# Performance work log

Measured on AMD Instinct MI355X. Metric: run time of the kernel, lower is better.

## Reference

```python
import jax, jax.numpy as jnp
import numpy as np

NEG_SLOPE = 0.2  # PyG GATConv default


def gat_conv(x, src, dst, W, att_src, att_dst, bias, n_nodes):
    # x: [N, F_in]; W: [F_in, H*C]; att_*: [H, C]; bias: [H*C]
    H, C = att_src.shape
    h = (x @ W).reshape(n_nodes, H, C)                      # [N, H, C]
    a_src = jnp.sum(h * att_src, axis=-1)                   # [N, H]
    a_dst = jnp.sum(h * att_dst, axis=-1)                   # [N, H]
    e = jax.nn.leaky_relu(a_src[src] + a_dst[dst], NEG_SLOPE)  # [E, H]
    # segment softmax over incoming edges of each dst node
    e_max = jax.ops.segment_max(e, dst, num_segments=n_nodes)
    e_max = jnp.where(jnp.isfinite(e_max), e_max, 0.0)
    ex = jnp.exp(e - e_max[dst])                             # [E, H]
    denom = jax.ops.segment_sum(ex, dst, num_segments=n_nodes)
    alpha = ex / (denom[dst] + 1e-16)                        # [E, H]
    msg = h[src] * alpha[:, :, None]                         # [E, H, C]
    out = jax.ops.segment_sum(msg, dst, num_segments=n_nodes)  # [N, H, C]
    return out.reshape(n_nodes, H * C) + bias


def setup_inputs() -> dict:
    key = jax.random.key(0)
    ks = jax.random.split(key, 12)
    N, F_in, Hd, heads, F_out, E = 50000, 128, 32, 8, 16, 800000
    x = jax.random.normal(ks[0], (N, F_in), dtype=jnp.float32)
    edge_index = jax.random.randint(ks[1], (2, E), 0, N, dtype=jnp.int64)
    g = 0.1
    return {
        "x": x,
        "edge_index": edge_index,
        "W1": jax.random.normal(ks[2], (F_in, heads * Hd), dtype=jnp.float32) * g,
        "att_src1": jax.random.normal(ks[3], (heads, Hd), dtype=jnp.float32) * g,
        "att_dst1": jax.random.normal(ks[4], (heads, Hd), dtype=jnp.float32) * g,
        "b1": jnp.zeros((heads * Hd,), dtype=jnp.float32),
        "W2": jax.random.normal(ks[5], (heads * Hd, Hd), dtype=jnp.float32) * g,
        "att_src2": jax.random.normal(ks[6], (1, Hd), dtype=jnp.float32) * g,
        "att_dst2": jax.random.normal(ks[7], (1, Hd), dtype=jnp.float32) * g,
        "b2": jnp.zeros((Hd,), dtype=jnp.float32),
        "Wout": jax.random.normal(ks[8], (Hd, F_out), dtype=jnp.float32) * g,
        "bout": jnp.zeros((F_out,), dtype=jnp.float32),
    }


def reference(x, edge_index, W1, att_src1, att_dst1, b1, W2, att_src2, att_dst2, b2, Wout, bout):
    N = x.shape[0]
    # PyG GATConv adds self loops by default
    loops = jnp.arange(N, dtype=edge_index.dtype)
    src = jnp.concatenate([edge_index[0], loops])
    dst = jnp.concatenate([edge_index[1], loops])
    h = jax.nn.elu(gat_conv(x, src, dst, W1, att_src1, att_dst1, b1, N))
    # dropout is identity in eval mode
    h = jax.nn.elu(gat_conv(h, src, dst, W2, att_src2, att_dst2, b2, N))
    return h @ Wout + bout
```

## Files before the change

### kernel.cpp

```cpp
#include <hip/hip_runtime.h>
#include <math.h>

#define NEG_SLOPE 0.2f

typedef __attribute__((ext_vector_type(8))) short bfrag8;
typedef __attribute__((ext_vector_type(4))) float f4acc;

__device__ __forceinline__ float bflo(unsigned int u) {
  union { unsigned int i; float f; } c;
  c.i = u << 16;
  return c.f;
}
__device__ __forceinline__ float bfhi(unsigned int u) {
  union { unsigned int i; float f; } c;
  c.i = u & 0xFFFF0000u;
  return c.f;
}
__device__ __forceinline__ unsigned short f2bf(float f) {
  union { float f; unsigned int i; } c;
  c.f = f;
  unsigned int i = c.i;
  return (unsigned short)((i + 0x7FFFu + ((i >> 16) & 1u)) >> 16);
}


__global__ __launch_bounds__(256) void hist_kernel(const int* __restrict__ ei,
                                                   int* __restrict__ counts, int e) {
  int i = blockIdx.x * 256 + threadIdx.x;
  if (i < e) atomicAdd(&counts[ei[e + i]], 1);
}

#define SCAN_TILE 2048
__global__ __launch_bounds__(256) void scan1_kernel(const int* __restrict__ counts,
                                                    int* __restrict__ offsets,
                                                    int* __restrict__ bsum, int n) {
  __shared__ int wtot[4];
  int tid = threadIdx.x;
  int base = blockIdx.x * SCAN_TILE + tid * 8;
  int v[8];
#pragma unroll
  for (int k = 0; k < 8; ++k) v[k] = (base + k < n) ? counts[base + k] + 1 : 0;
#pragma unroll
  for (int k = 1; k < 8; ++k) v[k] += v[k - 1];
  int tsum = v[7];
  int lane = tid & 63;
  int w = tid >> 6;
  int ws = tsum;
#pragma unroll
  for (int off = 1; off < 64; off <<= 1) {
    int t = __shfl_up(ws, off, 64);
    if (lane >= off) ws += t;
  }
  if (lane == 63) wtot[w] = ws;
  __syncthreads();
  int woff = 0;
#pragma unroll
  for (int k = 0; k < 3; ++k)
    if (k < w) woff += wtot[k];
  int thrBase = woff + ws - tsum;
#pragma unroll
  for (int k = 0; k < 8; ++k)
    if (base + k < n) offsets[base + k] = thrBase + v[k];
  if (tid == 255) bsum[blockIdx.x] = woff + ws;
}

__global__ __launch_bounds__(256) void scan3_kernel(const int* __restrict__ counts,
                                                    int* __restrict__ offsets,
                                                    const int* __restrict__ bsum,
                                                    int* __restrict__ cursor,
                                                    int n, int nb) {
  __shared__ int pres[64];
  int tid = threadIdx.x;
  if (tid < 64) {
    int v = (tid < nb) ? bsum[tid] : 0;
#pragma unroll
    for (int off = 1; off < 64; off <<= 1) {
      int t = __shfl_up(v, off, 64);
      if ((tid & 63) >= off) v += t;
    }
    pres[tid] = v;
  }
  __syncthreads();
  int i = blockIdx.x * 256 + tid;
  if (i > n) return;
  if (i == n) {
    offsets[n] = pres[nb - 1];
    return;
  }
  int b = i >> 11;
  int pre = (b == 0) ? 0 : pres[b - 1];
  int excl = pre + offsets[i] - (counts[i] + 1);
  offsets[i] = excl;
  cursor[i] = excl;
}

__global__ __launch_bounds__(256) void fill_kernel(const int* __restrict__ ei,
                                                   int* __restrict__ cursor,
                                                   int* __restrict__ csr, int n, int e) {
  int i = blockIdx.x * 256 + threadIdx.x;
  if (i < e) {
    int s = ei[i];
    int d = ei[e + i];
    int pos = atomicAdd(&cursor[d], 1);
    csr[pos] = s;
  } else if (i < e + n) {
    int node = i - e;
    int pos = atomicAdd(&cursor[node], 1);
    csr[pos] = node;
  } else if (i < e + n + 64) {
    csr[i] = 0;
  }
}


__global__ __launch_bounds__(256) void wcast_kernel(const float* __restrict__ W1,
                                                    const float* __restrict__ W2,
                                                    unsigned short* __restrict__ w1t,
                                                    unsigned short* __restrict__ w2t) {
  int gid = blockIdx.x * 256 + threadIdx.x;
#pragma unroll
  for (int u = 0; u < 4; ++u) {
    int j = gid * 4 + u;
    if (j < 128 * 256) {
      int k = j >> 8, c = j & 255;
      w1t[c * 128 + k] = f2bf(W1[j]);
    } else if (j < 128 * 256 + 256 * 32) {
      int j2 = j - 128 * 256;
      int k = j2 >> 5, c = j2 & 31;
      w2t[c * 256 + k] = f2bf(W2[j2]);
    }
  }
}

__global__ __launch_bounds__(256) void xcast_kernel(const float* __restrict__ x,
                                                    unsigned short* __restrict__ xb,
                                                    int total) {
  int gid = blockIdx.x * 256 + threadIdx.x;
  int i = gid * 8;
  if (i >= total) return;
  float4 v0 = *(const float4*)(x + i);
  float4 v1 = *(const float4*)(x + i + 4);
  uint4 q;
  q.x = (unsigned int)f2bf(v0.x) | ((unsigned int)f2bf(v0.y) << 16);
  q.y = (unsigned int)f2bf(v0.z) | ((unsigned int)f2bf(v0.w) << 16);
  q.z = (unsigned int)f2bf(v1.x) | ((unsigned int)f2bf(v1.y) << 16);
  q.w = (unsigned int)f2bf(v1.z) | ((unsigned int)f2bf(v1.w) << 16);
  *(uint4*)(xb + i) = q;
}


__global__ __launch_bounds__(256) void gemm1_kernel(const unsigned short* __restrict__ xb,
                                                    const unsigned short* __restrict__ w1t,
                                                    const float* __restrict__ att_src,
                                                    const float* __restrict__ att_dst,
                                                    unsigned short* __restrict__ h1b,
                                                    float* __restrict__ as1,
                                                    float* __restrict__ ad1, int n) {
  int tid = threadIdx.x;
  int wave = tid >> 6, lane = tid & 63;
  int quad = lane >> 4, l16 = lane & 15;
  int row0 = blockIdx.x * 64 + wave * 16;
  int col0 = blockIdx.y * 128;
  int rowA = min(row0 + l16, n - 1);

  f4acc acc[8];
#pragma unroll
  for (int t = 0; t < 8; ++t) acc[t] = (f4acc)(0.f);

#pragma unroll
  for (int kc = 0; kc < 4; ++kc) {
    bfrag8 a = *(const bfrag8*)(xb + (size_t)rowA * 128 + kc * 32 + quad * 8);
#pragma unroll
    for (int t = 0; t < 8; ++t) {
      bfrag8 b = *(const bfrag8*)(w1t + (size_t)(col0 + t * 16 + l16) * 128 + kc * 32 + quad * 8);
      acc[t] = __builtin_amdgcn_mfma_f32_16x16x32_bf16(a, b, acc[t], 0, 0, 0);
    }
  }

#pragma unroll
  for (int r = 0; r < 4; ++r) {
    int gr = row0 + quad * 4 + r;
    if (gr < n) {
#pragma unroll
      for (int t = 0; t < 8; ++t)
        h1b[(size_t)gr * 256 + col0 + t * 16 + l16] = f2bf(acc[t][r]);
    }
  }

  float s1[4][4], s2[4][4];
#pragma unroll
  for (int r = 0; r < 4; ++r)
#pragma unroll
    for (int hl = 0; hl < 4; ++hl) { s1[r][hl] = 0.f; s2[r][hl] = 0.f; }
#pragma unroll
  for (int t = 0; t < 8; ++t) {
    float av = att_src[col0 + t * 16 + l16];
    float dv = att_dst[col0 + t * 16 + l16];
    int hl = t >> 1;
#pragma unroll
    for (int r = 0; r < 4; ++r) {
      s1[r][hl] += acc[t][r] * av;
      s2[r][hl] += acc[t][r] * dv;
    }
  }
#pragma unroll
  for (int r = 0; r < 4; ++r) {
#pragma unroll
    for (int hl = 0; hl < 4; ++hl) {
      float v1 = s1[r][hl], v2 = s2[r][hl];
      v1 += __shfl_xor(v1, 1); v1 += __shfl_xor(v1, 2);
      v1 += __shfl_xor(v1, 4); v1 += __shfl_xor(v1, 8);
      v2 += __shfl_xor(v2, 1); v2 += __shfl_xor(v2, 2);
      v2 += __shfl_xor(v2, 4); v2 += __shfl_xor(v2, 8);
      if (l16 == 0) {
        int gr = row0 + quad * 4 + r;
        if (gr < n) {
          int hg = (col0 >> 5) + hl;
          as1[(size_t)gr * 8 + hg] = v1;
          ad1[(size_t)gr * 8 + hg] = v2;
        }
      }
    }
  }
}


__global__ __launch_bounds__(256) void agg1_kernel(const unsigned short* __restrict__ h1b,
                                                   const float* __restrict__ as1,
                                                   const float* __restrict__ ad1,
                                                   const int* __restrict__ offsets,
                                                   const int* __restrict__ csr,
                                                   const float* __restrict__ bias,
                                                   unsigned short* __restrict__ h1ob, int n) {
  __shared__ float peLds[4 * 64 * 8];
  int gtid = blockIdx.x * 256 + threadIdx.x;
  int node = gtid >> 6;
  int lane = gtid & 63;
  if (node >= n) return;
  float* myPe = peLds + (threadIdx.x >> 6) * 512;
  int beg = offsets[node], end = offsets[node + 1];
  int deg = end - beg;
  int half = lane >> 5, sub = lane & 31, head = sub >> 2;

  float4 adv0 = ((const float4*)(ad1 + (size_t)node * 8))[0];
  float4 adv1 = ((const float4*)(ad1 + (size_t)node * 8))[1];
  float ad_[8] = {adv0.x, adv0.y, adv0.z, adv0.w, adv1.x, adv1.y, adv1.z, adv1.w};

  float l = 0.f;
  float a[8] = {};

  for (int c0 = 0; c0 < deg; c0 += 64) {
    int cnt = min(64, deg - c0);
    bool valid = (c0 + lane) < deg;
    int s = csr[beg + c0 + lane];
    {
      const float4* ap = (const float4*)(as1 + (size_t)s * 8);
      float4 r0 = ap[0], r1 = ap[1];
      float asv[8] = {r0.x, r0.y, r0.z, r0.w, r1.x, r1.y, r1.z, r1.w};
      float pv[8];
#pragma unroll
      for (int h = 0; h < 8; ++h) {
        float ev = asv[h] + ad_[h];
        ev = ev > 0.f ? ev : NEG_SLOPE * ev;
        pv[h] = valid ? __expf(ev) : 0.f;
      }
      *(float4*)&myPe[lane * 8 + 0] = make_float4(pv[0], pv[1], pv[2], pv[3]);
      *(float4*)&myPe[lane * 8 + 4] = make_float4(pv[4], pv[5], pv[6], pv[7]);
    }
#pragma unroll 2
    for (int j = 0; j < cnt; j += 2) {
      int e = j + half;
      int s2 = csr[beg + c0 + e];
      float pe = myPe[e * 8 + head];
      l += pe;
      uint4 hv = *(const uint4*)(h1b + (size_t)s2 * 256 + sub * 8);
      a[0] += pe * bflo(hv.x);
      a[1] += pe * bfhi(hv.x);
      a[2] += pe * bflo(hv.y);
      a[3] += pe * bfhi(hv.y);
      a[4] += pe * bflo(hv.z);
      a[5] += pe * bfhi(hv.z);
      a[6] += pe * bflo(hv.w);
      a[7] += pe * bfhi(hv.w);
    }
  }
  l += __shfl_xor(l, 32);
#pragma unroll
  for (int i = 0; i < 8; ++i) a[i] += __shfl_xor(a[i], 32);

  if (half == 0) {
    float inv = 1.f / (l + 1e-16f);
    const float4* bp = (const float4*)(bias + sub * 8);
    float4 b0 = bp[0], b1 = bp[1];
    float o[8];
    o[0] = a[0] * inv + b0.x;
    o[1] = a[1] * inv + b0.y;
    o[2] = a[2] * inv + b0.z;
    o[3] = a[3] * inv + b0.w;
    o[4] = a[4] * inv + b1.x;
    o[5] = a[5] * inv + b1.y;
    o[6] = a[6] * inv + b1.z;
    o[7] = a[7] * inv + b1.w;
    unsigned int q[4];
#pragma unroll
    for (int j = 0; j < 4; ++j) {
      float e0 = o[j * 2], e1 = o[j * 2 + 1];
      e0 = e0 > 0.f ? e0 : expm1f(e0);
      e1 = e1 > 0.f ? e1 : expm1f(e1);
      q[j] = (unsigned int)f2bf(e0) | ((unsigned int)f2bf(e1) << 16);
    }
    *(uint4*)(h1ob + (size_t)node * 256 + sub * 8) = make_uint4(q[0], q[1], q[2], q[3]);
  }
}


__global__ __launch_bounds__(256) void gemm2_kernel(const unsigned short* __restrict__ h1ob,
                                                    const unsigned short* __restrict__ w2t,
                                                    const float* __restrict__ att_src,
                                                    const float* __restrict__ att_dst,
                                                    unsigned short* __restrict__ h2b,
                                                    float* __restrict__ as2,
                                                    float* __restrict__ ad2, int n) {
  int tid = threadIdx.x;
  int wave = tid >> 6, lane = tid & 63;
  int quad = lane >> 4, l16 = lane & 15;
  int row0 = blockIdx.x * 64 + wave * 16;
  int rowA = min(row0 + l16, n - 1);

  f4acc acc[2];
  acc[0] = (f4acc)(0.f);
  acc[1] = (f4acc)(0.f);

#pragma unroll
  for (int kc = 0; kc < 8; ++kc) {
    bfrag8 a = *(const bfrag8*)(h1ob + (size_t)rowA * 256 + kc * 32 + quad * 8);
#pragma unroll
    for (int t = 0; t < 2; ++t) {
      bfrag8 b = *(const bfrag8*)(w2t + (size_t)(t * 16 + l16) * 256 + kc * 32 + quad * 8);
      acc[t] = __builtin_amdgcn_mfma_f32_16x16x32_bf16(a, b, acc[t], 0, 0, 0);
    }
  }

#pragma unroll
  for (int r = 0; r < 4; ++r) {
    int gr = row0 + quad * 4 + r;
    if (gr < n) {
      h2b[(size_t)gr * 32 + l16] = f2bf(acc[0][r]);
      h2b[(size_t)gr * 32 + 16 + l16] = f2bf(acc[1][r]);
    }
  }

  float s1[4], s2v[4];
#pragma unroll
  for (int r = 0; r < 4; ++r) { s1[r] = 0.f; s2v[r] = 0.f; }
#pragma unroll
  for (int t = 0; t < 2; ++t) {
    float av = att_src[t * 16 + l16];
    float dv = att_dst[t * 16 + l16];
#pragma unroll
    for (int r = 0; r < 4; ++r) {
      s1[r] += acc[t][r] * av;
      s2v[r] += acc[t][r] * dv;
    }
  }
#pragma unroll
  for (int r = 0; r < 4; ++r) {
    float v1 = s1[r], v2 = s2v[r];
    v1 += __shfl_xor(v1, 1); v1 += __shfl_xor(v1, 2);
    v1 += __shfl_xor(v1, 4); v1 += __shfl_xor(v1, 8);
    v2 += __shfl_xor(v2, 1); v2 += __shfl_xor(v2, 2);
    v2 += __shfl_xor(v2, 4); v2 += __shfl_xor(v2, 8);
    if (l16 == 0) {
      int gr = row0 + quad * 4 + r;
      if (gr < n) {
        as2[gr] = v1;
        ad2[gr] = v2;
      }
    }
  }
}


__global__ __launch_bounds__(256) void agg2_kernel(const unsigned short* __restrict__ h2b,
                                                   const float* __restrict__ as2,
                                                   const float* __restrict__ ad2,
                                                   const int* __restrict__ offsets,
                                                   const int* __restrict__ csr,
                                                   const float* __restrict__ bias,
                                                   const float* __restrict__ Wout,
                                                   const float* __restrict__ bout,
                                                   float* __restrict__ out, int n) {
  __shared__ float peLds[4 * 64];
  __shared__ float wLds[512];
  __shared__ float hrow[4][32];
  int tid = threadIdx.x;
  wLds[tid] = Wout[tid];
  wLds[tid + 256] = Wout[tid + 256];
  __syncthreads();

  int gtid = blockIdx.x * 256 + tid;
  int node = gtid >> 6;
  int lane = gtid & 63;
  if (node >= n) return;
  int wv = tid >> 6;
  float* myPe = peLds + wv * 64;
  float ad = ad2[node];
  int beg = offsets[node], end = offsets[node + 1];
  int deg = end - beg;
  int quarter = lane >> 4;
  int dsub = lane & 15;

  float l = 0.f, a0 = 0.f, a1 = 0.f;
  for (int c0 = 0; c0 < deg; c0 += 64) {
    int cnt = min(64, deg - c0);
    bool valid = (c0 + lane) < deg;
    int s = csr[beg + c0 + lane];
    float ev = as2[s] + ad;
    ev = ev > 0.f ? ev : NEG_SLOPE * ev;
    myPe[lane] = valid ? __expf(ev) : 0.f;
#pragma unroll 2
    for (int j = 0; j < cnt; j += 4) {
      int e = j + quarter;
      int s2 = csr[beg + c0 + e];
      float pe = myPe[e];
      l += pe;
      unsigned int hv = *(const unsigned int*)(h2b + (size_t)s2 * 32 + dsub * 2);
      a0 += pe * bflo(hv);
      a1 += pe * bfhi(hv);
    }
  }
  l += __shfl_xor(l, 16);
  l += __shfl_xor(l, 32);
  a0 += __shfl_xor(a0, 16);
  a1 += __shfl_xor(a1, 16);
  a0 += __shfl_xor(a0, 32);
  a1 += __shfl_xor(a1, 32);
  if (lane < 16) {
    float inv = 1.f / (l + 1e-16f);
    float o0 = a0 * inv + bias[dsub * 2];
    float o1 = a1 * inv + bias[dsub * 2 + 1];
    o0 = o0 > 0.f ? o0 : expm1f(o0);
    o1 = o1 > 0.f ? o1 : expm1f(o1);
    hrow[wv][dsub * 2] = o0;
    hrow[wv][dsub * 2 + 1] = o1;
  }
  if (lane < 16) {
    float s = bout[lane];
#pragma unroll
    for (int c = 0; c < 32; ++c) s += hrow[wv][c] * wLds[c * 16 + lane];
    out[(size_t)node * 16 + lane] = s;
  }
}


extern "C" void kernel_launch(void* const* d_in, const int* in_sizes, int n_in,
                              void* d_out, int out_size, void* d_ws, size_t ws_size,
                              hipStream_t stream) {
  const float* x        = (const float*)d_in[0];
  const int*   ei       = (const int*)d_in[1];
  const float* W1       = (const float*)d_in[2];
  const float* att_src1 = (const float*)d_in[3];
  const float* att_dst1 = (const float*)d_in[4];
  const float* b1       = (const float*)d_in[5];
  const float* W2       = (const float*)d_in[6];
  const float* att_src2 = (const float*)d_in[7];
  const float* att_dst2 = (const float*)d_in[8];
  const float* b2       = (const float*)d_in[9];
  const float* Wout     = (const float*)d_in[10];
  const float* bout     = (const float*)d_in[11];
  float* out = (float*)d_out;

  int n = in_sizes[0] / 128;
  int e = in_sizes[1] / 2;

  char* w = (char*)d_ws;
  unsigned short* h1b  = (unsigned short*)w; w += (size_t)n * 256 * 2;
  unsigned short* h1ob = (unsigned short*)w; w += (size_t)n * 256 * 2;
  unsigned short* xb   = (unsigned short*)w; w += (size_t)n * 128 * 2;
  unsigned short* h2b  = (unsigned short*)w; w += (size_t)n * 32 * 2;
  unsigned short* w1t  = (unsigned short*)w; w += (size_t)256 * 128 * 2;
  unsigned short* w2t  = (unsigned short*)w; w += (size_t)32 * 256 * 2;
  float* as1  = (float*)w; w += (size_t)n * 8 * 4;
  float* ad1  = (float*)w; w += (size_t)n * 8 * 4;
  float* as2  = (float*)w; w += (size_t)n * 4;
  float* ad2  = (float*)w; w += (size_t)n * 4;
  int* counts  = (int*)w; w += (size_t)n * 4;
  int* offsets = (int*)w; w += (size_t)(n + 16) * 4;
  int* cursor  = (int*)w; w += (size_t)n * 4;
  int* csr     = (int*)w; w += (size_t)(e + n + 64) * 4;
  int* bsum    = (int*)w; w += (size_t)256 * 4;

  int nb = (n + SCAN_TILE - 1) / SCAN_TILE;

  hipMemsetAsync(counts, 0, (size_t)n * 4, stream);
  hist_kernel<<<(e + 255) / 256, 256, 0, stream>>>(ei, counts, e);
  scan1_kernel<<<nb, 256, 0, stream>>>(counts, offsets, bsum, n);
  scan3_kernel<<<(n + 256) / 256, 256, 0, stream>>>(counts, offsets, bsum, cursor, n, nb);
  fill_kernel<<<(e + n + 64 + 255) / 256, 256, 0, stream>>>(ei, cursor, csr, n, e);

  wcast_kernel<<<40, 256, 0, stream>>>(W1, W2, w1t, w2t);
  xcast_kernel<<<(n * 128 / 8 + 255) / 256, 256, 0, stream>>>(x, xb, n * 128);

  gemm1_kernel<<<dim3((n + 63) / 64, 2), 256, 0, stream>>>(xb, w1t, att_src1, att_dst1,
                                                           h1b, as1, ad1, n);
  agg1_kernel<<<(n + 3) / 4, 256, 0, stream>>>(h1b, as1, ad1, offsets, csr, b1, h1ob, n);

  gemm2_kernel<<<(n + 63) / 64, 256, 0, stream>>>(h1ob, w2t, att_src2, att_dst2,
                                                  h2b, as2, ad2, n);
  agg2_kernel<<<(n + 3) / 4, 256, 0, stream>>>(h2b, as2, ad2, offsets, csr, b2,
                                               Wout, bout, out, n);
}
```

Baseline: 342.7 us.

## Fuse histogram and cast kernels, raise aggregation unroll, use fast ELU

Merges the degree histogram, the x-to-bf16 cast and the weight transpose-cast into one prep kernel, removing two kernel launches and letting the independent work overlap. Raises the unroll factor of the edge-gather loops in both aggregation kernels from 2 to 4 to keep more loads in flight. Replaces expm1f-based ELU with __expf(x)-1, which is cheaper but loses accuracy for small negative inputs. The larger unroll may raise register pressure in the aggregation kernels.

```diff
diff --git a/kernel.cpp b/kernel.cpp
--- a/kernel.cpp
+++ b/kernel.cpp
@@ -22,13 +22,53 @@
   unsigned int i = c.i;
   return (unsigned short)((i + 0x7FFFu + ((i >> 16) & 1u)) >> 16);
 }
-
-
-__global__ __launch_bounds__(256) void hist_kernel(const int* __restrict__ ei,
-                                                   int* __restrict__ counts, int e) {
-  int i = blockIdx.x * 256 + threadIdx.x;
-  if (i < e) atomicAdd(&counts[ei[e + i]], 1);
-}
+__device__ __forceinline__ float elu(float x) { return x > 0.f ? x : __expf(x) - 1.f; }
+
+
+__global__ __launch_bounds__(256) void prep_kernel(const int* __restrict__ ei,
+                                                   int* __restrict__ counts,
+                                                   const float* __restrict__ x,
+                                                   const float* __restrict__ W1,
+                                                   const float* __restrict__ W2,
+                                                   unsigned short* __restrict__ xb,
+                                                   unsigned short* __restrict__ w1t,
+                                                   unsigned short* __restrict__ w2t,
+                                                   int e, int xThreads, int totalx) {
+  int gid = blockIdx.x * 256 + threadIdx.x;
+  if (gid < e) {
+    atomicAdd(&counts[ei[e + gid]], 1);
+    return;
+  }
+  int g1 = gid - e;
+  if (g1 < xThreads) {
+    int i = g1 * 8;
+    if (i < totalx) {
+      float4 v0 = *(const float4*)(x + i);
+      float4 v1 = *(const float4*)(x + i + 4);
+      uint4 q;
+      q.x = (unsigned int)f2bf(v0.x) | ((unsigned int)f2bf(v0.y) << 16);
+      q.y = (unsigned int)f2bf(v0.z) | ((unsigned int)f2bf(v0.w) << 16);
+      q.z = (unsigned int)f2bf(v1.x) | ((unsigned int)f2bf(v1.y) << 16);
+      q.w = (unsigned int)f2bf(v1.z) | ((unsigned int)f2bf(v1.w) << 16);
+      *(uint4*)(xb + i) = q;
+    }
+    return;
+  }
+  int g2 = g1 - xThreads;
+#pragma unroll
+  for (int u = 0; u < 4; ++u) {
+    int j = g2 * 4 + u;
+    if (j < 128 * 256) {
+      int k = j >> 8, c = j & 255;
+      w1t[c * 128 + k] = f2bf(W1[j]);
+    } else if (j < 128 * 256 + 256 * 32) {
+      int j2 = j - 128 * 256;
+      int k = j2 >> 5, c = j2 & 31;
+      w2t[c * 256 + k] = f2bf(W2[j2]);
+    }
+  }
+}
+
 
 #define SCAN_TILE 2048
 __global__ __launch_bounds__(256) void scan1_kernel(const int* __restrict__ counts,
@@ -110,42 +150,6 @@
   } else if (i < e + n + 64) {
     csr[i] = 0;
   }
-}
-
-
-__global__ __launch_bounds__(256) void wcast_kernel(const float* __restrict__ W1,
-                                                    const float* __restrict__ W2,
-                                                    unsigned short* __restrict__ w1t,
-                                                    unsigned short* __restrict__ w2t) {
-  int gid = blockIdx.x * 256 + threadIdx.x;
-#pragma unroll
-  for (int u = 0; u < 4; ++u) {
-    int j = gid * 4 + u;
-    if (j < 128 * 256) {
-      int k = j >> 8, c = j & 255;
-      w1t[c * 128 + k] = f2bf(W1[j]);
-    } else if (j < 128 * 256 + 256 * 32) {
-      int j2 = j - 128 * 256;
-      int k = j2 >> 5, c = j2 & 31;
-      w2t[c * 256 + k] = f2bf(W2[j2]);
-    }
-  }
-}
-
-__global__ __launch_bounds__(256) void xcast_kernel(const float* __restrict__ x,
-                                                    unsigned short* __restrict__ xb,
-                                                    int total) {
-  int gid = blockIdx.x * 256 + threadIdx.x;
-  int i = gid * 8;
-  if (i >= total) return;
-  float4 v0 = *(const float4*)(x + i);
-  float4 v1 = *(const float4*)(x + i + 4);
-  uint4 q;
-  q.x = (unsigned int)f2bf(v0.x) | ((unsigned int)f2bf(v0.y) << 16);
-  q.y = (unsigned int)f2bf(v0.z) | ((unsigned int)f2bf(v0.w) << 16);
-  q.z = (unsigned int)f2bf(v1.x) | ((unsigned int)f2bf(v1.y) << 16);
-  q.w = (unsigned int)f2bf(v1.z) | ((unsigned int)f2bf(v1.w) << 16);
-  *(uint4*)(xb + i) = q;
 }
 
 
@@ -267,7 +271,7 @@
       *(float4*)&myPe[lane * 8 + 0] = make_float4(pv[0], pv[1], pv[2], pv[3]);
       *(float4*)&myPe[lane * 8 + 4] = make_float4(pv[4], pv[5], pv[6], pv[7]);
     }
-#pragma unroll 2
+#pragma unroll 4
     for (int j = 0; j < cnt; j += 2) {
       int e = j + half;
       int s2 = csr[beg + c0 + e];
@@ -293,22 +297,18 @@
     const float4* bp = (const float4*)(bias + sub * 8);
     float4 b0 = bp[0], b1 = bp[1];
     float o[8];
-    o[0] = a[0] * inv + b0.x;
-    o[1] = a[1] * inv + b0.y;
-    o[2] = a[2] * inv + b0.z;
-    o[3] = a[3] * inv + b0.w;
-    o[4] = a[4] * inv + b1.x;
-    o[5] = a[5] * inv + b1.y;
-    o[6] = a[6] * inv + b1.z;
-    o[7] = a[7] * inv + b1.w;
+    o[0] = elu(a[0] * inv + b0.x);
+    o[1] = elu(a[1] * inv + b0.y);
+    o[2] = elu(a[2] * inv + b0.z);
+    o[3] = elu(a[3] * inv + b0.w);
+    o[4] = elu(a[4] * inv + b1.x);
+    o[5] = elu(a[5] * inv + b1.y);
+    o[6] = elu(a[6] * inv + b1.z);
+    o[7] = elu(a[7] * inv + b1.w);
     unsigned int q[4];
 #pragma unroll
-    for (int j = 0; j < 4; ++j) {
-      float e0 = o[j * 2], e1 = o[j * 2 + 1];
-      e0 = e0 > 0.f ? e0 : expm1f(e0);
-      e1 = e1 > 0.f ? e1 : expm1f(e1);
-      q[j] = (unsigned int)f2bf(e0) | ((unsigned int)f2bf(e1) << 16);
-    }
+    for (int j = 0; j < 4; ++j)
+      q[j] = (unsigned int)f2bf(o[j * 2]) | ((unsigned int)f2bf(o[j * 2 + 1]) << 16);
     *(uint4*)(h1ob + (size_t)node * 256 + sub * 8) = make_uint4(q[0], q[1], q[2], q[3]);
   }
 }
@@ -418,7 +418,7 @@
     float ev = as2[s] + ad;
     ev = ev > 0.f ? ev : NEG_SLOPE * ev;
     myPe[lane] = valid ? __expf(ev) : 0.f;
-#pragma unroll 2
+#pragma unroll 4
     for (int j = 0; j < cnt; j += 4) {
       int e = j + quarter;
       int s2 = csr[beg + c0 + e];
@@ -437,10 +437,8 @@
   a1 += __shfl_xor(a1, 32);
   if (lane < 16) {
     float inv = 1.f / (l + 1e-16f);
-    float o0 = a0 * inv + bias[dsub * 2];
-    float o1 = a1 * inv + bias[dsub * 2 + 1];
-    o0 = o0 > 0.f ? o0 : expm1f(o0);
-    o1 = o1 > 0.f ? o1 : expm1f(o1);
+    float o0 = elu(a0 * inv + bias[dsub * 2]);
+    float o1 = elu(a1 * inv + bias[dsub * 2 + 1]);
     hrow[wv][dsub * 2] = o0;
     hrow[wv][dsub * 2 + 1] = o1;
   }
@@ -493,13 +491,15 @@
   int nb = (n + SCAN_TILE - 1) / SCAN_TILE;
 
   hipMemsetAsync(counts, 0, (size_t)n * 4, stream);
-  hist_kernel<<<(e + 255) / 256, 256, 0, stream>>>(ei, counts, e);
+  int xThreads = (n * 128 + 7) / 8;
+  int prepThreads = e + xThreads + (128 * 256 + 256 * 32 + 3) / 4;
+  prep_kernel<<<(prepThreads + 255) / 256, 256, 0, stream>>>(ei, counts, x, W1, W2,
+                                                             xb, w1t, w2t, e, xThreads,
+                                                             n * 128);
+
   scan1_kernel<<<nb, 256, 0, stream>>>(counts, offsets, bsum, n);
   scan3_kernel<<<(n + 256) / 256, 256, 0, stream>>>(counts, offsets, bsum, cursor, n, nb);
   fill_kernel<<<(e + n + 64 + 255) / 256, 256, 0, stream>>>(ei, cursor, csr, n, e);
-
-  wcast_kernel<<<40, 256, 0, stream>>>(W1, W2, w1t, w2t);
-  xcast_kernel<<<(n * 128 / 8 + 255) / 256, 256, 0, stream>>>(x, xb, n * 128);
 
   gemm1_kernel<<<dim3((n + 63) / 64, 2), 256, 0, stream>>>(xb, w1t, att_src1, att_dst1,
                                                            h1b, as1, ad1, n);
```

New measurement: 334.5 us. 1.02x faster.
